# Performance work log

Measured on AMD Instinct MI355X. Metric: run time of the kernel, lower is better.

Reference implementation:

```python
import jax, jax.numpy as jnp
import numpy as np

N_GROUP = 8
TOPK_GROUP = 4
TOP_K = 8
ROUTED_SCALING = 2.5
NUM_EXPERTS = 256
HIDDEN = 7168
TOKENS = 8192


def setup_inputs() -> dict:
    key = jax.random.key(0)
    k1, k2, k3 = jax.random.split(key, 3)
    hidden_states = jax.random.normal(k1, (TOKENS, HIDDEN), dtype=jnp.float32)
    weight = jax.random.normal(k2, (NUM_EXPERTS, HIDDEN), dtype=jnp.float32) * 0.02
    e_score_correction_bias = jax.random.normal(k3, (NUM_EXPERTS,), dtype=jnp.float32) * 0.1
    return {"hidden_states": hidden_states, "weight": weight,
            "e_score_correction_bias": e_score_correction_bias}


def reference(hidden_states, weight, e_score_correction_bias):
    # logits = x @ W^T  (fp32 gate GEMM)
    logits = jnp.einsum('th,eh->te', hidden_states.astype(jnp.float32), weight)
    scores = jax.nn.sigmoid(logits)                       # [T, E]
    swb = scores + e_score_correction_bias                # [T, E]
    T, E = swb.shape
    gsize = E // N_GROUP
    # per-group score = sum of top-2 biased scores within each group
    grouped = swb.reshape(T, N_GROUP, gsize)
    top2, _ = jax.lax.top_k(grouped, 2)                   # [T, G, 2]
    group_scores = top2.sum(axis=-1)                      # [T, G]
    # keep topk_group groups
    _, gidx = jax.lax.top_k(group_scores, TOPK_GROUP)     # [T, topk_group]
    rows = jnp.arange(T)[:, None]
    group_mask = jnp.zeros((T, N_GROUP), jnp.float32).at[rows, gidx].set(1.0)
    score_mask = jnp.repeat(group_mask, gsize, axis=-1)   # [T, E]
    swb_masked = swb * score_mask
    # top_k experts among kept groups
    _, tidx = jax.lax.top_k(swb_masked, TOP_K)            # [T, top_k]
    new_mask = jnp.zeros((T, E), jnp.float32).at[rows, tidx].set(1.0)
    sel = scores * new_mask
    score_sum = sel.sum(axis=-1, keepdims=True) + 1e-20
    return sel / score_sum * ROUTED_SCALING
```

## Files before the change

### kernel.cpp

```cpp
#include <hip/hip_runtime.h>
#include <math.h>

#define TOKENS   8192
#define HIDDEN   7168
#define NEXPERT  256
#define NGROUP   8
#define TOPKG    4
#define TOPK     8
#define SCALE    2.5f

#define BM 128
#define BN 128
#define BK 32
#define KSPLIT 4
#define KPB (HIDDEN / KSPLIT)
#define NT  (KPB / BK)

#define RSTR 72

typedef _Float16 half8 __attribute__((ext_vector_type(8)));
typedef _Float16 half4 __attribute__((ext_vector_type(4)));
typedef float    floatx4 __attribute__((ext_vector_type(4)));

__device__ __forceinline__ void cvt_store(_Float16* __restrict__ H,
                                          int row, int k0, float4 v) {
    half4 h, l;
    h[0] = (_Float16)v.x; h[1] = (_Float16)v.y;
    h[2] = (_Float16)v.z; h[3] = (_Float16)v.w;
    l[0] = (_Float16)(v.x - (float)h[0]);
    l[1] = (_Float16)(v.y - (float)h[1]);
    l[2] = (_Float16)(v.z - (float)h[2]);
    l[3] = (_Float16)(v.w - (float)h[3]);
    const int base = row * RSTR + ((k0 >> 3) << 4) + (k0 & 7);
    *(half4*)&H[base]     = h;
    *(half4*)&H[base + 8] = l;
}

__global__ __launch_bounds__(256) void zero_kernel(float* __restrict__ O) {
    const int i = blockIdx.x * 256 + threadIdx.x;
    *(float4*)&O[(size_t)i * 4] = float4{0.f, 0.f, 0.f, 0.f};
}

__global__ __launch_bounds__(256, 2) void gate_gemm_kernel(
    const float* __restrict__ X, const float* __restrict__ W,
    float* __restrict__ OUT)
{
    __shared__ _Float16 Ab[2][BM * RSTR];
    __shared__ _Float16 Bb[2][BN * RSTR];

    const int tid = threadIdx.x;
    const int nb  = blockIdx.x * BN;
    const int mb  = blockIdx.y * BM;
    const int kb  = blockIdx.z * KPB;

    const int srow = tid >> 3;
    const int sk0  = (tid & 7) * 4;
    const float* Aptr = X + (size_t)(mb + srow) * HIDDEN + kb + sk0;
    const float* Bptr = W + (size_t)(nb + srow) * HIDDEN + kb + sk0;

    const int lane = tid & 63, wave = tid >> 6;
    const int wm = (wave >> 1) * 64, wn = (wave & 1) * 64;
    const int fr = lane & 15, quad = lane >> 4;

    floatx4 acc[4][4];
#pragma unroll
    for (int i = 0; i < 4; i++)
#pragma unroll
        for (int j = 0; j < 4; j++) acc[i][j] = floatx4{0.f, 0.f, 0.f, 0.f};

    float4 av0[4], bv0[4], av1[4], bv1[4];

    auto load_tile = [&](float4* av, float4* bv, int t) {
        const int o = t * BK;
#pragma unroll
        for (int q = 0; q < 4; q++) {
            av[q] = *(const float4*)(Aptr + o + (size_t)(q * 32) * HIDDEN);
            bv[q] = *(const float4*)(Bptr + o + (size_t)(q * 32) * HIDDEN);
        }
    };
    auto stage = [&](_Float16* A, _Float16* B, const float4* av,
                     const float4* bv) {
#pragma unroll
        for (int q = 0; q < 4; q++) {
            cvt_store(A, q * 32 + srow, sk0, av[q]);
            cvt_store(B, q * 32 + srow, sk0, bv[q]);
        }
    };
    auto compute = [&](const _Float16* __restrict__ Ac,
                       const _Float16* __restrict__ Bc) {
        half8 ah[4], al[4];
#pragma unroll
        for (int i = 0; i < 4; i++) {
            const int a = (wm + i * 16 + fr) * RSTR + quad * 16;
            ah[i] = *(const half8*)&Ac[a];
            al[i] = *(const half8*)&Ac[a + 8];
        }
#pragma unroll
        for (int j = 0; j < 4; j++) {
            const int b = (wn + j * 16 + fr) * RSTR + quad * 16;
            const half8 bh = *(const half8*)&Bc[b];
            const half8 bl = *(const half8*)&Bc[b + 8];
#pragma unroll
            for (int i = 0; i < 4; i++) {
                acc[i][j] = __builtin_amdgcn_mfma_f32_16x16x32_f16(
                    al[i], bh, acc[i][j], 0, 0, 0);
                acc[i][j] = __builtin_amdgcn_mfma_f32_16x16x32_f16(
                    ah[i], bl, acc[i][j], 0, 0, 0);
                acc[i][j] = __builtin_amdgcn_mfma_f32_16x16x32_f16(
                    ah[i], bh, acc[i][j], 0, 0, 0);
            }
        }
    };

    load_tile(av0, bv0, 0);
    load_tile(av1, bv1, 1);
    stage(Ab[0], Bb[0], av0, bv0);

#pragma unroll 1
    for (int t = 0; t < NT; t += 2) {
        __syncthreads();
        if (t + 2 < NT) load_tile(av0, bv0, t + 2);
        compute(Ab[0], Bb[0]);
        stage(Ab[1], Bb[1], av1, bv1);

        __syncthreads();
        if (t + 3 < NT) load_tile(av1, bv1, t + 3);
        compute(Ab[1], Bb[1]);
        if (t + 2 < NT) stage(Ab[0], Bb[0], av0, bv0);
    }

#pragma unroll
    for (int i = 0; i < 4; i++)
#pragma unroll
        for (int j = 0; j < 4; j++) {
            const int col = nb + wn + j * 16 + fr;
#pragma unroll
            for (int r = 0; r < 4; r++) {
                const int row = mb + wm + i * 16 + quad * 4 + r;
                atomicAdd(&OUT[(size_t)row * NEXPERT + col], acc[i][j][r]);
            }
        }
}

__global__ __launch_bounds__(256) void route_kernel(
    float* __restrict__ S, const float* __restrict__ bias)
{
    const int lane = threadIdx.x & 63;
    const int wave = threadIdx.x >> 6;
    const int t    = blockIdx.x * 4 + wave;

    const float4 lg4 = *(const float4*)&S[(size_t)t * NEXPERT + lane * 4];
    const float4 b4  = *(const float4*)&bias[lane * 4];
    float sc[4];
    sc[0] = 1.0f / (1.0f + expf(-lg4.x));
    sc[1] = 1.0f / (1.0f + expf(-lg4.y));
    sc[2] = 1.0f / (1.0f + expf(-lg4.z));
    sc[3] = 1.0f / (1.0f + expf(-lg4.w));
    float swb[4] = { sc[0] + b4.x, sc[1] + b4.y, sc[2] + b4.z, sc[3] + b4.w };

    float m1 = -INFINITY, m2 = -INFINITY;
#pragma unroll
    for (int j = 0; j < 4; j++) {
        const float v = swb[j];
        if (v > m1)      { m2 = m1; m1 = v; }
        else if (v > m2) { m2 = v; }
    }
#pragma unroll
    for (int s = 1; s < 8; s <<= 1) {
        const float o1 = __shfl_xor(m1, s, 64);
        const float o2 = __shfl_xor(m2, s, 64);
        const float hi = fmaxf(m1, o1);
        const float lo = fminf(m1, o1);
        m2 = fmaxf(lo, fmaxf(m2, o2));
        m1 = hi;
    }
    const float gs = m1 + m2;

    float gsc[NGROUP];
#pragma unroll
    for (int g = 0; g < NGROUP; g++) gsc[g] = __shfl(gs, g * 8, 64);
    const int myg = lane >> 3;
    int rank = 0;
#pragma unroll
    for (int g = 0; g < NGROUP; g++)
        rank += (gsc[g] > gs) || (gsc[g] == gs && g < myg);
    const bool kept = (rank < TOPKG);

    float v[4];
#pragma unroll
    for (int j = 0; j < 4; j++) v[j] = kept ? swb[j] : 0.0f;

    float sum = 0.0f;
    int selmask = 0;
    for (int r = 0; r < TOPK; r++) {
        float bv = -INFINITY;
        int   bi = 0x7fffffff;
#pragma unroll
        for (int j = 0; j < 4; j++) {
            const bool avail = ((selmask >> j) & 1) == 0;
            if (avail && v[j] > bv) { bv = v[j]; bi = lane * 4 + j; }
        }
#pragma unroll
        for (int s = 1; s < 64; s <<= 1) {
            const float ov = __shfl_xor(bv, s, 64);
            const int   oi = __shfl_xor(bi, s, 64);
            if (ov > bv || (ov == bv && oi < bi)) { bv = ov; bi = oi; }
        }
        const int wl = bi >> 2, wj = bi & 3;
        const float mysc = (wj == 0) ? sc[0] : (wj == 1) ? sc[1]
                         : (wj == 2) ? sc[2] : sc[3];
        sum += __shfl(mysc, wl, 64);
        if (lane == wl) selmask |= (1 << wj);
    }

    const float rcp = SCALE / (sum + 1e-20f);
    float4 o;
    o.x = (selmask & 1) ? sc[0] * rcp : 0.0f;
    o.y = (selmask & 2) ? sc[1] * rcp : 0.0f;
    o.z = (selmask & 4) ? sc[2] * rcp : 0.0f;
    o.w = (selmask & 8) ? sc[3] * rcp : 0.0f;
    *(float4*)&S[(size_t)t * NEXPERT + lane * 4] = o;
}

extern "C" void kernel_launch(void* const* d_in, const int* in_sizes, int n_in,
                              void* d_out, int out_size, void* d_ws, size_t ws_size,
                              hipStream_t stream) {
    const float* X    = (const float*)d_in[0];
    const float* W    = (const float*)d_in[1];
    const float* bias = (const float*)d_in[2];
    float* out = (float*)d_out;
    (void)d_ws; (void)ws_size;

    zero_kernel<<<(TOKENS * NEXPERT / 4) / 256, 256, 0, stream>>>(out);
    dim3 ggrid(NEXPERT / BN, TOKENS / BM, KSPLIT);
    gate_gemm_kernel<<<ggrid, 256, 0, stream>>>(X, W, out);
    route_kernel<<<TOKENS / 4, 256, 0, stream>>>(out, bias);
}
```

Before: 385.7 us.

## Single-buffer split hi/lo LDS planes, double K-split, raise occupancy to 3

Moves the fp16 high and low halves into separate LDS planes with a tighter row stride, and drops the LDS double buffer so shared memory per block shrinks. Prefetching now uses one register set instead of two. KSPLIT doubles to 8 and launch bounds ask for 3 blocks per CU, aiming to add parallelism and hide latency through occupancy. The cost is a second barrier per K-step, less load/compute overlap, and twice as many atomicAdd operations on the output.

```diff
diff --git a/kernel.cpp b/kernel.cpp
--- a/kernel.cpp
+++ b/kernel.cpp
@@ -12,17 +12,19 @@
 #define BM 128
 #define BN 128
 #define BK 32
-#define KSPLIT 4
+#define KSPLIT 8
 #define KPB (HIDDEN / KSPLIT)
 #define NT  (KPB / BK)
 
-#define RSTR 72
+#define RSTR  40
+#define PLANE (BM * RSTR)
 
 typedef _Float16 half8 __attribute__((ext_vector_type(8)));
 typedef _Float16 half4 __attribute__((ext_vector_type(4)));
 typedef float    floatx4 __attribute__((ext_vector_type(4)));
 
-__device__ __forceinline__ void cvt_store(_Float16* __restrict__ H,
+__device__ __forceinline__ void cvt_store(_Float16* __restrict__ Hh,
+                                          _Float16* __restrict__ Hl,
                                           int row, int k0, float4 v) {
     half4 h, l;
     h[0] = (_Float16)v.x; h[1] = (_Float16)v.y;
@@ -31,9 +33,9 @@
     l[1] = (_Float16)(v.y - (float)h[1]);
     l[2] = (_Float16)(v.z - (float)h[2]);
     l[3] = (_Float16)(v.w - (float)h[3]);
-    const int base = row * RSTR + ((k0 >> 3) << 4) + (k0 & 7);
-    *(half4*)&H[base]     = h;
-    *(half4*)&H[base + 8] = l;
+    const int a = row * RSTR + k0;
+    *(half4*)&Hh[a] = h;
+    *(half4*)&Hl[a] = l;
 }
 
 __global__ __launch_bounds__(256) void zero_kernel(float* __restrict__ O) {
@@ -41,12 +43,15 @@
     *(float4*)&O[(size_t)i * 4] = float4{0.f, 0.f, 0.f, 0.f};
 }
 
-__global__ __launch_bounds__(256, 2) void gate_gemm_kernel(
+__global__ __launch_bounds__(256, 3) void gate_gemm_kernel(
     const float* __restrict__ X, const float* __restrict__ W,
     float* __restrict__ OUT)
 {
-    __shared__ _Float16 Ab[2][BM * RSTR];
-    __shared__ _Float16 Bb[2][BN * RSTR];
+    __shared__ _Float16 S[4 * PLANE];
+    _Float16* __restrict__ Ah = S;
+    _Float16* __restrict__ Al = S + PLANE;
+    _Float16* __restrict__ Bh = S + 2 * PLANE;
+    _Float16* __restrict__ Bl = S + 3 * PLANE;
 
     const int tid = threadIdx.x;
     const int nb  = blockIdx.x * BN;
@@ -68,9 +73,9 @@
 #pragma unroll
         for (int j = 0; j < 4; j++) acc[i][j] = floatx4{0.f, 0.f, 0.f, 0.f};
 
-    float4 av0[4], bv0[4], av1[4], bv1[4];
-
-    auto load_tile = [&](float4* av, float4* bv, int t) {
+    float4 av[4], bv[4];
+
+    auto load_tile = [&](int t) {
         const int o = t * BK;
 #pragma unroll
         for (int q = 0; q < 4; q++) {
@@ -78,28 +83,26 @@
             bv[q] = *(const float4*)(Bptr + o + (size_t)(q * 32) * HIDDEN);
         }
     };
-    auto stage = [&](_Float16* A, _Float16* B, const float4* av,
-                     const float4* bv) {
+    auto stage = [&]() {
 #pragma unroll
         for (int q = 0; q < 4; q++) {
-            cvt_store(A, q * 32 + srow, sk0, av[q]);
-            cvt_store(B, q * 32 + srow, sk0, bv[q]);
+            cvt_store(Ah, Al, q * 32 + srow, sk0, av[q]);
+            cvt_store(Bh, Bl, q * 32 + srow, sk0, bv[q]);
         }
     };
-    auto compute = [&](const _Float16* __restrict__ Ac,
-                       const _Float16* __restrict__ Bc) {
+    auto compute = [&]() {
         half8 ah[4], al[4];
 #pragma unroll
         for (int i = 0; i < 4; i++) {
-            const int a = (wm + i * 16 + fr) * RSTR + quad * 16;
-            ah[i] = *(const half8*)&Ac[a];
-            al[i] = *(const half8*)&Ac[a + 8];
+            const int a = (wm + i * 16 + fr) * RSTR + quad * 8;
+            ah[i] = *(const half8*)&Ah[a];
+            al[i] = *(const half8*)&Al[a];
         }
 #pragma unroll
         for (int j = 0; j < 4; j++) {
-            const int b = (wn + j * 16 + fr) * RSTR + quad * 16;
-            const half8 bh = *(const half8*)&Bc[b];
-            const half8 bl = *(const half8*)&Bc[b + 8];
+            const int b = (wn + j * 16 + fr) * RSTR + quad * 8;
+            const half8 bh = *(const half8*)&Bh[b];
+            const half8 bl = *(const half8*)&Bl[b];
 #pragma unroll
             for (int i = 0; i < 4; i++) {
                 acc[i][j] = __builtin_amdgcn_mfma_f32_16x16x32_f16(
@@ -112,21 +115,16 @@
         }
     };
 
-    load_tile(av0, bv0, 0);
-    load_tile(av1, bv1, 1);
-    stage(Ab[0], Bb[0], av0, bv0);
+    load_tile(0);
+    stage();
 
 #pragma unroll 1
-    for (int t = 0; t < NT; t += 2) {
+    for (int t = 0; t < NT; t++) {
         __syncthreads();
-        if (t + 2 < NT) load_tile(av0, bv0, t + 2);
-        compute(Ab[0], Bb[0]);
-        stage(Ab[1], Bb[1], av1, bv1);
-
+        if (t + 1 < NT) load_tile(t + 1);
+        compute();
         __syncthreads();
-        if (t + 3 < NT) load_tile(av1, bv1, t + 3);
-        compute(Ab[1], Bb[1]);
-        if (t + 2 < NT) stage(Ab[0], Bb[0], av0, bv0);
+        if (t + 1 < NT) stage();
     }
 
 #pragma unroll
```

After: 396.2 us. 1.03x slower.
